# Performance work log

Hardware: AMD Instinct MI355X
Metric: run time of the kernel (lower is better)

## Reference

```python
import jax, jax.numpy as jnp
import numpy as np

NX = NY = 128
N = NX * NY            # 16384 tiles
F = 26                 # in_feats
H = 512                # hidden_dim
NH = 8                 # heads
HD = H // NH           # head_dim = 64
DEPTH = 4
LN_EPS = 1e-5


def _grid_edge_index(nx, ny):
    """4-connected grid, bidirectional edges (src, dst) like _build_grid_edge_index."""
    idx = np.arange(nx * ny).reshape(nx, ny)
    hs, hd = idx[:, :-1].ravel(), idx[:, 1:].ravel()   # horizontal neighbors
    vs, vd = idx[:-1, :].ravel(), idx[1:, :].ravel()   # vertical neighbors
    src = np.concatenate([hs, hd, vs, vd]).astype(np.int32)
    dst = np.concatenate([hd, hs, vd, vs]).astype(np.int32)
    return src, dst


def setup_inputs() -> dict:
    key = jax.random.key(0)
    ks = jax.random.split(key, 8)
    s = 0.02
    src, dst = _grid_edge_index(NX, NY)
    return {
        "graph": jax.random.normal(ks[0], (N, F), jnp.float32),
        "edge_src": jnp.asarray(src),
        "edge_dst": jnp.asarray(dst),
        "Wp": jax.random.normal(ks[1], (F, H), jnp.float32) * s,
        "bp": jnp.zeros((H,), jnp.float32),
        "Wq": jax.random.normal(ks[2], (DEPTH, H, H), jnp.float32) * s,
        "bq": jnp.zeros((DEPTH, H), jnp.float32),
        "Wk": jax.random.normal(ks[3], (DEPTH, H, H), jnp.float32) * s,
        "bk": jnp.zeros((DEPTH, H), jnp.float32),
        "Wv": jax.random.normal(ks[4], (DEPTH, H, H), jnp.float32) * s,
        "bv": jnpp_zeros((DEPTH, H)) if False else jnp.zeros((DEPTH, H), jnp.float32),
        "Ws": jax.random.normal(ks[5], (DEPTH, H, H), jnp.float32) * s,
        "bs": jnp.zeros((DEPTH, H), jnp.float32),
        "Wbeta": jax.random.normal(ks[6], (DEPTH, 3 * H), jnp.float32) * s,
        "ln_g": jnp.ones((DEPTH, H), jnp.float32),
        "ln_b": jnp.zeros((DEPTH, H), jnp.float32),
    }


def _layernorm(x, g, b):
    mu = x.mean(-1, keepdims=True)
    var = ((x - mu) ** 2).mean(-1, keepdims=True)
    return (x - mu) * jax.lax.rsqrt(var + LN_EPS) * g + b


def _transformer_conv(x, src, dst, Wq, bq, Wk, bk, Wv, bv, Ws, bs, Wbeta):
    n = x.shape[0]
    q = (x @ Wq + bq).reshape(n, NH, HD)
    k = (x @ Wk + bk).reshape(n, NH, HD)
    v = (x @ Wv + bv).reshape(n, NH, HD)
    # per-edge attention logits: query at target (dst), key at source (src)
    alpha = (q[dst] * k[src]).sum(-1) / jnp.sqrt(jnp.float32(HD))  # (E, NH)
    # segment softmax over incoming edges of each target node (PyG softmax)
    m = jax.ops.segment_max(alpha, dst, num_segments=n)
    e = jnp.exp(alpha - m[dst])
    denom = jax.ops.segment_sum(e, dst, num_segments=n)
    a = e / (denom[dst] + 1e-16)
    # beta-gated scatter-add aggregation
    out = jax.ops.segment_sum(a[:, :, None] * v[src], dst, num_segments=n)
    out = out.reshape(n, H)
    r = x @ Ws + bs                                  # root/skip projection
    g = jax.nn.sigmoid(jnp.concatenate([out, r, out - r], -1) @ Wbeta)  # (n,)
    g = g[:, None]
    return g * r + (1.0 - g) * out


def reference(graph, edge_src, edge_dst, Wp, bp, Wq, bq, Wk, bk, Wv, bv,
              Ws, bs, Wbeta, ln_g, ln_b):
    x = graph @ Wp + bp
    for l in range(DEPTH):
        h = _transformer_conv(x, edge_src, edge_dst, Wq[l], bq[l], Wk[l], bk[l],
                              Wv[l], bv[l], Ws[l], bs[l], Wbeta[l])
        x = _layernorm(x + h, ln_g[l], ln_b[l])
    global_emb = x.mean(0, keepdims=True)
    return (x, global_emb)


def jnp_zeros(shape):  # unused helper guard
    return jnp.zeros(shape, jnp.float32)

jnp_p_zeros = None

def jnp_zeros_unused():
    pass

# fix accidental typo-safe alias used in setup_inputs
jnp_zeros_f = jnp.zeros

def jnp_noop():
    pass

jnp_zeros2 = jnp.zeros

def jnp_p_zeros_fn(shape):
    return jnp.zeros(shape, jnp.float32)

jnp_p_zeros = jnp_p_zeros_fn

def jnp_zeros3(shape):
    return jnp.zeros(shape, jnp.float32)

jnp_p = jnp

def jnp_zeros4(shape):
    return jnp.zeros(shape, jnp.float32)

jnp_zeros5 = jnp.zeros

def jnp_zeros6(shape):
    return jnp.zeros(shape, jnp.float32)

jnp_p_zeros_alias = jnp.zeros

def jnp_p_zeros_(shape):
    return jnp.zeros(shape, jnp.float32)

jnp_p_zeros__ = jnp.zeros

# alias referenced defensively inside setup_inputs (never called)
jnp_p_zeros___ = jnp.zeros

def jnp_p_zeros____(shape):
    return jnp.zeros(shape, jnp.float32)

jnp_p_zeros_____ = jnp.zeros

jnp_p_zeros______ = jnp.zeros

jnp_p_zeros_______ = jnp.zeros

jnp_p_zeros________ = jnp.zeros

jnp_p_zeros_________ = jnp.zeros

jnp_p_zeros__________ = jnp.zeros

# name used in the dead branch of setup_inputs
jnp_p_zeros = jnp.zeros

def jnp_p_zeros_def(shape):
    return jnp.zeros(shape, jnp.float32)

jnpp_zeros = jnp.zeros
```

## Files before the change

kernel.cpp:

```cpp
#include <hip/hip_runtime.h>
#include <hip/hip_bf16.h>
#include <math.h>

#define NN    16384
#define FF    26
#define HH    512
#define NHEAD 8
#define HDIM  64
#define GRID_W 128
#define LN_EPS 1e-5f

typedef __attribute__((ext_vector_type(8))) short short8;
typedef __attribute__((ext_vector_type(4))) float f32x4;
typedef __attribute__((ext_vector_type(4))) short s16x4;

static __device__ __forceinline__ float bf2f(short u) {
  unsigned int x = ((unsigned int)(unsigned short)u) << 16;
  return __uint_as_float(x);
}
static __device__ __forceinline__ short f2bf(float f) {
  __hip_bfloat16 h = __float2bfloat16(f);
  return __builtin_bit_cast(short, h);
}
static __device__ __forceinline__ float dot8(short8 a, short8 b) {
  float p = 0.f;
#pragma unroll
  for (int j = 0; j < 8; ++j) p += bf2f(a[j]) * bf2f(b[j]);
  return p;
}

__global__ __launch_bounds__(256) void wconv_kernel(
    const float* __restrict__ Wq, const float* __restrict__ Wk,
    const float* __restrict__ Wv, const float* __restrict__ Ws,
    __hip_bfloat16* __restrict__ Wt) {
  __shared__ float ls[32][33];
  int bid = blockIdx.x;
  int mi = bid >> 8, kt = (bid >> 4) & 15, nt = bid & 15;
  int l = mi >> 2, m = mi & 3;
  const float* src = ((m == 0) ? Wq : (m == 1) ? Wk : (m == 2) ? Wv : Ws)
                   + (size_t)l * 262144;
  int c = threadIdx.x & 31, r = threadIdx.x >> 5;
#pragma unroll
  for (int p = 0; p < 4; ++p)
    ls[r + 8 * p][c] = src[(size_t)(kt * 32 + r + 8 * p) * 512 + nt * 32 + c];
  __syncthreads();
#pragma unroll
  for (int p = 0; p < 4; ++p)
    Wt[((size_t)mi * 512 + nt * 32 + r + 8 * p) * 512 + kt * 32 + c] =
        __float2bfloat16(ls[c][r + 8 * p]);
}

__global__ __launch_bounds__(256) void bconv_kernel(
    const float* __restrict__ bq, const float* __restrict__ bk,
    const float* __restrict__ bv, const float* __restrict__ bs,
    float* __restrict__ bcat) {
  int tid = blockIdx.x * 256 + threadIdx.x;
  int j = tid & 511;
  int m = (tid >> 9) & 3;
  int l = tid >> 11;
  const float* src = (m == 0) ? bq : (m == 1) ? bk : (m == 2) ? bv : bs;
  bcat[tid] = src[l * 512 + j];
}

__global__ __launch_bounds__(256) void gconv_kernel(
    const float* __restrict__ graph, __hip_bfloat16* __restrict__ gb) {
  int tid = blockIdx.x * 256 + threadIdx.x;
  int n = tid >> 5, k = tid & 31;
  gb[tid] = __float2bfloat16(k < FF ? graph[n * FF + k] : 0.f);
}

__global__ __launch_bounds__(256) void wpconv_kernel(
    const float* __restrict__ Wp, __hip_bfloat16* __restrict__ Wpt) {
  int tid = blockIdx.x * 256 + threadIdx.x;
  int j = tid >> 5, k = tid & 31;
  Wpt[tid] = __float2bfloat16(k < FF ? Wp[k * HH + j] : 0.f);
}

template <int LDA, int KDIM, int LDC, bool WF32, bool REPACK>
__global__ __launch_bounds__(256) void gemm_t(
    const __hip_bfloat16* __restrict__ A,
    const __hip_bfloat16* __restrict__ Bt,
    const float* __restrict__ bias,
    __hip_bfloat16* __restrict__ C,
    float* __restrict__ Xf) {
  __shared__ __align__(16) char lds[16384];
  const int t    = threadIdx.x;
  const int wv   = t >> 6;
  const int lane = t & 63;
  const int m0 = blockIdx.x * 128, n0 = blockIdx.y * 128;

  const int srow = (wv << 4) + (lane >> 2);
  const int gch  = (lane & 3) ^ ((lane >> 3) & 3);
  const char* agp = (const char*)(A  + (size_t)(m0 + srow) * LDA + (gch << 3));
  const char* bgp = (const char*)(Bt + (size_t)(n0 + srow) * KDIM + (gch << 3));
  char* aldst = lds +        (wv << 10) + (lane << 4);
  char* bldst = lds + 8192 + (wv << 10) + (lane << 4);

  const int q  = lane >> 4;
  const int r  = lane & 15;
  const int fs = (r >> 1) & 3;
  const int ksl = ((q ^ fs) << 4);
  const int wm = wv >> 1, wn = wv & 1;
  int aoff[4], boff[4];
#pragma unroll
  for (int i = 0; i < 4; ++i) {
    aoff[i] = (((wm << 6) + (i << 4) + r) << 6) + ksl;
    boff[i] = 8192 + (((wn << 6) + (i << 4) + r) << 6) + ksl;
  }

  f32x4 acc[4][4];
#pragma unroll
  for (int i = 0; i < 4; ++i)
#pragma unroll
    for (int j = 0; j < 4; ++j) acc[i][j] = (f32x4){0.f, 0.f, 0.f, 0.f};

  for (int k0 = 0; k0 < KDIM; k0 += 32) {
    __syncthreads();
    const size_t kb = (size_t)k0 * 2;
    __builtin_amdgcn_global_load_lds(
        (const __attribute__((address_space(1))) void*)(agp + kb),
        (__attribute__((address_space(3))) void*)(aldst), 16, 0, 0);
    __builtin_amdgcn_global_load_lds(
        (const __attribute__((address_space(1))) void*)(agp + kb + (size_t)LDA * 128),
        (__attribute__((address_space(3))) void*)(aldst + 4096), 16, 0, 0);
    __builtin_amdgcn_global_load_lds(
        (const __attribute__((address_space(1))) void*)(bgp + kb),
        (__attribute__((address_space(3))) void*)(bldst), 16, 0, 0);
    __builtin_amdgcn_global_load_lds(
        (const __attribute__((address_space(1))) void*)(bgp + kb + (size_t)KDIM * 128),
        (__attribute__((address_space(3))) void*)(bldst + 4096), 16, 0, 0);
    __syncthreads();

    short8 af[4], bfr[4];
#pragma unroll
    for (int i = 0; i < 4; ++i) af[i]  = *(const short8*)(lds + aoff[i]);
#pragma unroll
    for (int i = 0; i < 4; ++i) bfr[i] = *(const short8*)(lds + boff[i]);
#pragma unroll
    for (int mi = 0; mi < 4; ++mi)
#pragma unroll
      for (int ni = 0; ni < 4; ++ni)
        acc[mi][ni] = __builtin_amdgcn_mfma_f32_16x16x32_bf16(
            af[mi], bfr[ni], acc[mi][ni], 0, 0, 0);
  }

  if (REPACK) {
    const int S = 136;
    short* lp = (short*)lds;
#pragma unroll
    for (int mi = 0; mi < 4; ++mi) {
      __syncthreads();
#pragma unroll
      for (int ni = 0; ni < 4; ++ni) {
        const int col = (wn << 6) + (ni << 4) + r;
        const float bb = bias[n0 + col];
#pragma unroll
        for (int e = 0; e < 4; ++e)
          lp[((wm << 4) + (q << 2) + e) * S + col] = f2bf(acc[mi][ni][e] + bb);
      }
      __syncthreads();
#pragma unroll
      for (int s2 = 0; s2 < 2; ++s2) {
        const int slot = t + (s2 << 8);
        const int rl = slot >> 4, seg = slot & 15;
        short8 vseg = *(const short8*)(lp + rl * S + (seg << 3));
        const int grow = m0 + ((rl >> 4) << 6) + (mi << 4) + (rl & 15);
        *(short8*)(C + (size_t)grow * LDC + n0 + (seg << 3)) = vseg;
      }
    }
  } else {
#pragma unroll
    for (int ni = 0; ni < 4; ++ni) {
      const int col = n0 + (wn << 6) + (ni << 4) + r;
      const float bb = bias[col];
#pragma unroll
      for (int mi = 0; mi < 4; ++mi) {
        const size_t rb = (size_t)(m0 + (wm << 6) + (mi << 4) + (q << 2));
#pragma unroll
        for (int e = 0; e < 4; ++e) {
          float val = acc[mi][ni][e] + bb;
          C[(rb + e) * LDC + col] = __float2bfloat16(val);
          if (WF32) Xf[(rb + e) * LDC + col] = val;
        }
      }
    }
  }
}

__global__ __launch_bounds__(128) void node_kernel(
    const __hip_bfloat16* __restrict__ qkvs,
    float* __restrict__ x, __hip_bfloat16* __restrict__ xb,
    const float* __restrict__ Wb, const float* __restrict__ lng,
    const float* __restrict__ lnb) {
  int n = blockIdx.x;
  int t = threadIdx.x;
  __shared__ float s_alpha[32];
  __shared__ float s_aw[32];
  __shared__ float redA[2], redB[2], redC[2];

  const int gi = n >> 7, gj = n & 127;
  int nbr[4];
  nbr[0] = (gj > 0)          ? n - 1      : -1;
  nbr[1] = (gj < GRID_W - 1) ? n + 1      : -1;
  nbr[2] = (gi > 0)          ? n - GRID_W : -1;
  nbr[3] = (gi < GRID_W - 1) ? n + GRID_W : -1;

  {
    const int e = t >> 5, h = (t >> 2) & 7, sub = t & 3;
    const int me = (nbr[e] >= 0) ? nbr[e] : n;
    const short8* qp = (const short8*)(qkvs + (size_t)n * 2048 + h * 64 + sub * 16);
    const short8* kp = (const short8*)(qkvs + (size_t)me * 2048 + 512 + h * 64 + sub * 16);
    float p = dot8(qp[0], kp[0]) + dot8(qp[1], kp[1]);
    p += __shfl_xor(p, 1);
    p += __shfl_xor(p, 2);
    if (sub == 0) s_alpha[e * 8 + h] = p * 0.125f;
  }
  __syncthreads();

  if (t < 8) {
    float a[4];
#pragma unroll
    for (int e = 0; e < 4; ++e) a[e] = (nbr[e] >= 0) ? s_alpha[e * 8 + t] : -1e30f;
    float mx = fmaxf(fmaxf(a[0], a[1]), fmaxf(a[2], a[3]));
    float ee[4];
    float sum = 1e-16f;
#pragma unroll
    for (int e = 0; e < 4; ++e) {
      ee[e] = (nbr[e] >= 0) ? expf(a[e] - mx) : 0.f;
      sum += ee[e];
    }
    float inv = 1.f / sum;
#pragma unroll
    for (int e = 0; e < 4; ++e) s_aw[t * 4 + e] = ee[e] * inv;
  }
  __syncthreads();

  const int c0 = t << 2;
  const int h  = c0 >> 6;

  float4 ov = make_float4(0.f, 0.f, 0.f, 0.f);
#pragma unroll
  for (int e = 0; e < 4; ++e) {
    int m = nbr[e];
    if (m >= 0) {
      float a = s_aw[h * 4 + e];
      s16x4 vv = *(const s16x4*)(qkvs + (size_t)m * 2048 + 1024 + c0);
      ov.x += a * bf2f(vv[0]); ov.y += a * bf2f(vv[1]);
      ov.z += a * bf2f(vv[2]); ov.w += a * bf2f(vv[3]);
    }
  }
  s16x4 rr = *(const s16x4*)(qkvs + (size_t)n * 2048 + 1536 + c0);
  float4 rv = make_float4(bf2f(rr[0]), bf2f(rr[1]), bf2f(rr[2]), bf2f(rr[3]));

  float4 w0 = *(const float4*)(Wb + c0);
  float4 w1 = *(const float4*)(Wb + 512 + c0);
  float4 w2 = *(const float4*)(Wb + 1024 + c0);
  float part = ov.x * w0.x + ov.y * w0.y + ov.z * w0.z + ov.w * w0.w
             + rv.x * w1.x + rv.y * w1.y + rv.z * w1.z + rv.w * w1.w
             + (ov.x - rv.x) * w2.x + (ov.y - rv.y) * w2.y
             + (ov.z - rv.z) * w2.z + (ov.w - rv.w) * w2.w;
#pragma unroll
  for (int s = 32; s > 0; s >>= 1) part += __shfl_xor(part, s);
  int wv = t >> 6, ln = t & 63;
  if (ln == 0) redA[wv] = part;
  __syncthreads();
  float g = 1.f / (1.f + expf(-(redA[0] + redA[1])));

  float4 xv = *(const float4*)(x + (size_t)n * HH + c0);
  float4 y;
  y.x = xv.x + g * rv.x + (1.f - g) * ov.x;
  y.y = xv.y + g * rv.y + (1.f - g) * ov.y;
  y.z = xv.z + g * rv.z + (1.f - g) * ov.z;
  y.w = xv.w + g * rv.w + (1.f - g) * ov.w;

  float s1 = y.x + y.y + y.z + y.w;
  float sq = y.x * y.x + y.y * y.y + y.z * y.z + y.w * y.w;
#pragma unroll
  for (int s = 32; s > 0; s >>= 1) {
    s1 += __shfl_xor(s1, s);
    sq += __shfl_xor(sq, s);
  }
  if (ln == 0) { redB[wv] = s1; redC[wv] = sq; }
  __syncthreads();
  float S1 = redB[0] + redB[1], S2 = redC[0] + redC[1];
  float mu  = S1 * (1.f / 512.f);
  float var = S2 * (1.f / 512.f) - mu * mu;
  float rs  = rsqrtf(var + LN_EPS);

  float4 gg = *(const float4*)(lng + c0);
  float4 bb = *(const float4*)(lnb + c0);
  float4 o;
  o.x = (y.x - mu) * rs * gg.x + bb.x;
  o.y = (y.y - mu) * rs * gg.y + bb.y;
  o.z = (y.z - mu) * rs * gg.z + bb.z;
  o.w = (y.w - mu) * rs * gg.w + bb.w;
  *(float4*)(x + (size_t)n * HH + c0) = o;
  s16x4 ob;
  ob[0] = f2bf(o.x); ob[1] = f2bf(o.y); ob[2] = f2bf(o.z); ob[3] = f2bf(o.w);
  *(s16x4*)(xb + (size_t)n * HH + c0) = ob;
}

__global__ void zero_kernel(float* __restrict__ p) { p[threadIdx.x] = 0.f; }

__global__ __launch_bounds__(512) void col_mean_kernel(
    const float* __restrict__ x, float* __restrict__ g) {
  int t  = threadIdx.x;
  int n0 = blockIdx.x * 256;
  float s = 0.f;
  for (int rr = 0; rr < 256; ++rr) s += x[(size_t)(n0 + rr) * HH + t];
  atomicAdd(&g[t], s * (1.f / 16384.f));
}

extern "C" void kernel_launch(void* const* d_in, const int* in_sizes, int n_in,
                              void* d_out, int out_size, void* d_ws, size_t ws_size,
                              hipStream_t stream) {
  const float* graph = (const float*)d_in[0];
  const float* Wp = (const float*)d_in[3];
  const float* bp = (const float*)d_in[4];
  const float* Wq = (const float*)d_in[5];
  const float* bq = (const float*)d_in[6];
  const float* Wk = (const float*)d_in[7];
  const float* bk = (const float*)d_in[8];
  const float* Wv = (const float*)d_in[9];
  const float* bv = (const float*)d_in[10];
  const float* Wst = (const float*)d_in[11];
  const float* bst = (const float*)d_in[12];
  const float* Wbeta = (const float*)d_in[13];
  const float* lng = (const float*)d_in[14];
  const float* lnb = (const float*)d_in[15];

  float* x = (float*)d_out;
  char* ws = (char*)d_ws;
  __hip_bfloat16* qkvs = (__hip_bfloat16*)ws;
  __hip_bfloat16* xb   = (__hip_bfloat16*)(ws + 67108864);
  __hip_bfloat16* Wt   = (__hip_bfloat16*)(ws + 83886080);
  __hip_bfloat16* gb   = (__hip_bfloat16*)(ws + 92274688);
  __hip_bfloat16* Wpt  = (__hip_bfloat16*)(ws + 93323264);
  float* bcat          = (float*)(ws + 93356032);

  wconv_kernel<<<4096, 256, 0, stream>>>(Wq, Wk, Wv, Wst, Wt);
  bconv_kernel<<<32, 256, 0, stream>>>(bq, bk, bv, bst, bcat);
  gconv_kernel<<<NN * 32 / 256, 256, 0, stream>>>(graph, gb);
  wpconv_kernel<<<64, 256, 0, stream>>>(Wp, Wpt);

  gemm_t<32, 32, 512, true, false><<<dim3(128, 4), 256, 0, stream>>>(
      gb, Wpt, bp, xb, x);

  for (int l = 0; l < 4; ++l) {
    gemm_t<512, 512, 2048, false, true><<<dim3(128, 16), 256, 0, stream>>>(
        xb, Wt + (size_t)l * 4 * 262144, bcat + l * 2048, qkvs, nullptr);
    node_kernel<<<NN, 128, 0, stream>>>(qkvs, x, xb,
        Wbeta + (size_t)l * 1536, lng + (size_t)l * 512, lnb + (size_t)l * 512);
  }

  zero_kernel<<<1, 512, 0, stream>>>(x + (size_t)NN * HH);
  col_mean_kernel<<<64, 512, 0, stream>>>(x, x + (size_t)NN * HH);
}
```

Baseline: 448.6 us.

## Use per-wave GEMM epilogue repack and one-wave-per-node attention kernel

The GEMM epilogue now repacks each wave's 16x64 tile through its own LDS region and writes 16-byte rows. This replaces the block-wide repack, which needed a __syncthreads per row group. The node kernel maps one 64-lane wave to each node, with four nodes arranged as a 2x2 grid patch per block, so every reduction is done with wave shuffles and no LDS or barriers. The goal is to remove synchronisation overhead, widen loads to 8 bf16 per lane, and improve neighbour locality. The per-wave LDS repack uses a 66-element stride, which may cause bank conflicts.

```diff
diff --git a/kernel.cpp b/kernel.cpp
--- a/kernel.cpp
+++ b/kernel.cpp
@@ -76,7 +76,7 @@
   Wpt[tid] = __float2bfloat16(k < FF ? Wp[k * HH + j] : 0.f);
 }
 
-template <int LDA, int KDIM, int LDC, bool WF32, bool REPACK>
+template <int LDA, int KDIM, int LDC, bool WF32>
 __global__ __launch_bounds__(256) void gemm_t(
     const __hip_bfloat16* __restrict__ A,
     const __hip_bfloat16* __restrict__ Bt,
@@ -144,160 +144,151 @@
             af[mi], bfr[ni], acc[mi][ni], 0, 0, 0);
   }
 
-  if (REPACK) {
-    const int S = 136;
-    short* lp = (short*)lds;
-#pragma unroll
-    for (int mi = 0; mi < 4; ++mi) {
-      __syncthreads();
+  float bbv[4];
+#pragma unroll
+  for (int ni = 0; ni < 4; ++ni) bbv[ni] = bias[n0 + (wn << 6) + (ni << 4) + r];
+
+  __syncthreads();
+
+  short* lp = (short*)(lds + (wv << 12));
+  const int rl = lane >> 2, sg = lane & 3;
+#pragma unroll
+  for (int mi = 0; mi < 4; ++mi) {
+#pragma unroll
+    for (int ni = 0; ni < 4; ++ni)
+#pragma unroll
+      for (int e = 0; e < 4; ++e)
+        lp[((q << 2) + e) * 66 + (ni << 4) + r] = f2bf(acc[mi][ni][e] + bbv[ni]);
+    const short* rp = lp + rl * 66 + (sg << 4);
+    short8 v0 = *(const short8*)rp;
+    short8 v1 = *(const short8*)(rp + 8);
+    const int grow = m0 + (wm << 6) + (mi << 4) + rl;
+    short8* cp = (short8*)(C + (size_t)grow * LDC + n0 + (wn << 6) + (sg << 4));
+    cp[0] = v0;
+    cp[1] = v1;
+    if (WF32) {
 #pragma unroll
       for (int ni = 0; ni < 4; ++ni) {
-        const int col = (wn << 6) + (ni << 4) + r;
-        const float bb = bias[n0 + col];
+        const int col = n0 + (wn << 6) + (ni << 4) + r;
+        const size_t rb = (size_t)(m0 + (wm << 6) + (mi << 4) + (q << 2));
 #pragma unroll
         for (int e = 0; e < 4; ++e)
-          lp[((wm << 4) + (q << 2) + e) * S + col] = f2bf(acc[mi][ni][e] + bb);
-      }
-      __syncthreads();
-#pragma unroll
-      for (int s2 = 0; s2 < 2; ++s2) {
-        const int slot = t + (s2 << 8);
-        const int rl = slot >> 4, seg = slot & 15;
-        short8 vseg = *(const short8*)(lp + rl * S + (seg << 3));
-        const int grow = m0 + ((rl >> 4) << 6) + (mi << 4) + (rl & 15);
-        *(short8*)(C + (size_t)grow * LDC + n0 + (seg << 3)) = vseg;
+          Xf[(rb + e) * LDC + col] = acc[mi][ni][e] + bbv[ni];
       }
     }
-  } else {
-#pragma unroll
-    for (int ni = 0; ni < 4; ++ni) {
-      const int col = n0 + (wn << 6) + (ni << 4) + r;
-      const float bb = bias[col];
-#pragma unroll
-      for (int mi = 0; mi < 4; ++mi) {
-        const size_t rb = (size_t)(m0 + (wm << 6) + (mi << 4) + (q << 2));
-#pragma unroll
-        for (int e = 0; e < 4; ++e) {
-          float val = acc[mi][ni][e] + bb;
-          C[(rb + e) * LDC + col] = __float2bfloat16(val);
-          if (WF32) Xf[(rb + e) * LDC + col] = val;
-        }
-      }
-    }
-  }
-}
-
-__global__ __launch_bounds__(128) void node_kernel(
+  }
+}
+
+__global__ __launch_bounds__(256) void node_kernel(
     const __hip_bfloat16* __restrict__ qkvs,
     float* __restrict__ x, __hip_bfloat16* __restrict__ xb,
     const float* __restrict__ Wb, const float* __restrict__ lng,
     const float* __restrict__ lnb) {
-  int n = blockIdx.x;
-  int t = threadIdx.x;
-  __shared__ float s_alpha[32];
-  __shared__ float s_aw[32];
-  __shared__ float redA[2], redB[2], redC[2];
-
-  const int gi = n >> 7, gj = n & 127;
+  const int t = threadIdx.x;
+  const int wv = t >> 6, lane = t & 63;
+  const int bi = blockIdx.x;
+  const int gi = ((bi >> 6) << 1) + (wv >> 1);
+  const int gj = ((bi & 63) << 1) + (wv & 1);
+  const int n = (gi << 7) + gj;
+
   int nbr[4];
   nbr[0] = (gj > 0)          ? n - 1      : -1;
   nbr[1] = (gj < GRID_W - 1) ? n + 1      : -1;
   nbr[2] = (gi > 0)          ? n - GRID_W : -1;
   nbr[3] = (gi < GRID_W - 1) ? n + GRID_W : -1;
 
-  {
-    const int e = t >> 5, h = (t >> 2) & 7, sub = t & 3;
+  const int c0 = lane << 3;
+
+  short8 q8 = *(const short8*)(qkvs + (size_t)n * 2048 + c0);
+  float al[4];
+#pragma unroll
+  for (int e = 0; e < 4; ++e) {
     const int me = (nbr[e] >= 0) ? nbr[e] : n;
-    const short8* qp = (const short8*)(qkvs + (size_t)n * 2048 + h * 64 + sub * 16);
-    const short8* kp = (const short8*)(qkvs + (size_t)me * 2048 + 512 + h * 64 + sub * 16);
-    float p = dot8(qp[0], kp[0]) + dot8(qp[1], kp[1]);
+    short8 k8 = *(const short8*)(qkvs + (size_t)me * 2048 + 512 + c0);
+    float p = dot8(q8, k8);
     p += __shfl_xor(p, 1);
     p += __shfl_xor(p, 2);
-    if (sub == 0) s_alpha[e * 8 + h] = p * 0.125f;
-  }
-  __syncthreads();
-
-  if (t < 8) {
-    float a[4];
-#pragma unroll
-    for (int e = 0; e < 4; ++e) a[e] = (nbr[e] >= 0) ? s_alpha[e * 8 + t] : -1e30f;
-    float mx = fmaxf(fmaxf(a[0], a[1]), fmaxf(a[2], a[3]));
-    float ee[4];
-    float sum = 1e-16f;
-#pragma unroll
-    for (int e = 0; e < 4; ++e) {
-      ee[e] = (nbr[e] >= 0) ? expf(a[e] - mx) : 0.f;
-      sum += ee[e];
+    p += __shfl_xor(p, 4);
+    al[e] = (nbr[e] >= 0) ? p * 0.125f : -1e30f;
+  }
+  float mx = fmaxf(fmaxf(al[0], al[1]), fmaxf(al[2], al[3]));
+  float aw[4], sum = 1e-16f;
+#pragma unroll
+  for (int e = 0; e < 4; ++e) {
+    aw[e] = (nbr[e] >= 0) ? expf(al[e] - mx) : 0.f;
+    sum += aw[e];
+  }
+  float inv = 1.f / sum;
+#pragma unroll
+  for (int e = 0; e < 4; ++e) aw[e] *= inv;
+
+  float ov[8] = {0.f, 0.f, 0.f, 0.f, 0.f, 0.f, 0.f, 0.f};
+#pragma unroll
+  for (int e = 0; e < 4; ++e) {
+    if (nbr[e] >= 0) {
+      short8 v8 = *(const short8*)(qkvs + (size_t)nbr[e] * 2048 + 1024 + c0);
+#pragma unroll
+      for (int j = 0; j < 8; ++j) ov[j] += aw[e] * bf2f(v8[j]);
     }
-    float inv = 1.f / sum;
-#pragma unroll
-    for (int e = 0; e < 4; ++e) s_aw[t * 4 + e] = ee[e] * inv;
-  }
-  __syncthreads();
-
-  const int c0 = t << 2;
-  const int h  = c0 >> 6;
-
-  float4 ov = make_float4(0.f, 0.f, 0.f, 0.f);
-#pragma unroll
-  for (int e = 0; e < 4; ++e) {
-    int m = nbr[e];
-    if (m >= 0) {
-      float a = s_aw[h * 4 + e];
-      s16x4 vv = *(const s16x4*)(qkvs + (size_t)m * 2048 + 1024 + c0);
-      ov.x += a * bf2f(vv[0]); ov.y += a * bf2f(vv[1]);
-      ov.z += a * bf2f(vv[2]); ov.w += a * bf2f(vv[3]);
-    }
-  }
-  s16x4 rr = *(const s16x4*)(qkvs + (size_t)n * 2048 + 1536 + c0);
-  float4 rv = make_float4(bf2f(rr[0]), bf2f(rr[1]), bf2f(rr[2]), bf2f(rr[3]));
-
-  float4 w0 = *(const float4*)(Wb + c0);
-  float4 w1 = *(const float4*)(Wb + 512 + c0);
-  float4 w2 = *(const float4*)(Wb + 1024 + c0);
-  float part = ov.x * w0.x + ov.y * w0.y + ov.z * w0.z + ov.w * w0.w
-             + rv.x * w1.x + rv.y * w1.y + rv.z * w1.z + rv.w * w1.w
-             + (ov.x - rv.x) * w2.x + (ov.y - rv.y) * w2.y
-             + (ov.z - rv.z) * w2.z + (ov.w - rv.w) * w2.w;
+  }
+  short8 s8 = *(const short8*)(qkvs + (size_t)n * 2048 + 1536 + c0);
+  float rv[8];
+#pragma unroll
+  for (int j = 0; j < 8; ++j) rv[j] = bf2f(s8[j]);
+
+  const float4* w0p = (const float4*)(Wb + c0);
+  const float4* w1p = (const float4*)(Wb + 512 + c0);
+  const float4* w2p = (const float4*)(Wb + 1024 + c0);
+  float4 w0a = w0p[0], w0b = w0p[1];
+  float4 w1a = w1p[0], w1b = w1p[1];
+  float4 w2a = w2p[0], w2b = w2p[1];
+  float w0[8] = {w0a.x, w0a.y, w0a.z, w0a.w, w0b.x, w0b.y, w0b.z, w0b.w};
+  float w1[8] = {w1a.x, w1a.y, w1a.z, w1a.w, w1b.x, w1b.y, w1b.z, w1b.w};
+  float w2[8] = {w2a.x, w2a.y, w2a.z, w2a.w, w2b.x, w2b.y, w2b.z, w2b.w};
+  float part = 0.f;
+#pragma unroll
+  for (int j = 0; j < 8; ++j)
+    part += ov[j] * w0[j] + rv[j] * w1[j] + (ov[j] - rv[j]) * w2[j];
 #pragma unroll
   for (int s = 32; s > 0; s >>= 1) part += __shfl_xor(part, s);
-  int wv = t >> 6, ln = t & 63;
-  if (ln == 0) redA[wv] = part;
-  __syncthreads();
-  float g = 1.f / (1.f + expf(-(redA[0] + redA[1])));
-
-  float4 xv = *(const float4*)(x + (size_t)n * HH + c0);
-  float4 y;
-  y.x = xv.x + g * rv.x + (1.f - g) * ov.x;
-  y.y = xv.y + g * rv.y + (1.f - g) * ov.y;
-  y.z = xv.z + g * rv.z + (1.f - g) * ov.z;
-  y.w = xv.w + g * rv.w + (1.f - g) * ov.w;
-
-  float s1 = y.x + y.y + y.z + y.w;
-  float sq = y.x * y.x + y.y * y.y + y.z * y.z + y.w * y.w;
+  float g = 1.f / (1.f + expf(-part));
+
+  const float4* xp = (const float4*)(x + (size_t)n * HH + c0);
+  float4 xa = xp[0], xc = xp[1];
+  float xv[8] = {xa.x, xa.y, xa.z, xa.w, xc.x, xc.y, xc.z, xc.w};
+  float y[8], s1 = 0.f, sq = 0.f;
+#pragma unroll
+  for (int j = 0; j < 8; ++j) {
+    y[j] = xv[j] + g * rv[j] + (1.f - g) * ov[j];
+    s1 += y[j];
+    sq += y[j] * y[j];
+  }
 #pragma unroll
   for (int s = 32; s > 0; s >>= 1) {
     s1 += __shfl_xor(s1, s);
     sq += __shfl_xor(sq, s);
   }
-  if (ln == 0) { redB[wv] = s1; redC[wv] = sq; }
-  __syncthreads();
-  float S1 = redB[0] + redB[1], S2 = redC[0] + redC[1];
-  float mu  = S1 * (1.f / 512.f);
-  float var = S2 * (1.f / 512.f) - mu * mu;
+  float mu  = s1 * (1.f / 512.f);
+  float var = sq * (1.f / 512.f) - mu * mu;
   float rs  = rsqrtf(var + LN_EPS);
 
-  float4 gg = *(const float4*)(lng + c0);
-  float4 bb = *(const float4*)(lnb + c0);
-  float4 o;
-  o.x = (y.x - mu) * rs * gg.x + bb.x;
-  o.y = (y.y - mu) * rs * gg.y + bb.y;
-  o.z = (y.z - mu) * rs * gg.z + bb.z;
-  o.w = (y.w - mu) * rs * gg.w + bb.w;
-  *(float4*)(x + (size_t)n * HH + c0) = o;
-  s16x4 ob;
-  ob[0] = f2bf(o.x); ob[1] = f2bf(o.y); ob[2] = f2bf(o.z); ob[3] = f2bf(o.w);
-  *(s16x4*)(xb + (size_t)n * HH + c0) = ob;
+  const float4* gp = (const float4*)(lng + c0);
+  const float4* bp = (const float4*)(lnb + c0);
+  float4 ga = gp[0], gc = gp[1];
+  float4 ba = bp[0], bc = bp[1];
+  float gg[8] = {ga.x, ga.y, ga.z, ga.w, gc.x, gc.y, gc.z, gc.w};
+  float bb[8] = {ba.x, ba.y, ba.z, ba.w, bc.x, bc.y, bc.z, bc.w};
+  float o[8];
+  short8 ob;
+#pragma unroll
+  for (int j = 0; j < 8; ++j) {
+    o[j] = (y[j] - mu) * rs * gg[j] + bb[j];
+    ob[j] = f2bf(o[j]);
+  }
+  float4* xo = (float4*)(x + (size_t)n * HH + c0);
+  xo[0] = make_float4(o[0], o[1], o[2], o[3]);
+  xo[1] = make_float4(o[4], o[5], o[6], o[7]);
+  *(short8*)(xb + (size_t)n * HH + c0) = ob;
 }
 
 __global__ void zero_kernel(float* __restrict__ p) { p[threadIdx.x] = 0.f; }
@@ -343,13 +334,13 @@
   gconv_kernel<<<NN * 32 / 256, 256, 0, stream>>>(graph, gb);
   wpconv_kernel<<<64, 256, 0, stream>>>(Wp, Wpt);
 
-  gemm_t<32, 32, 512, true, false><<<dim3(128, 4), 256, 0, stream>>>(
+  gemm_t<32, 32, 512, true><<<dim3(128, 4), 256, 0, stream>>>(
       gb, Wpt, bp, xb, x);
 
   for (int l = 0; l < 4; ++l) {
-    gemm_t<512, 512, 2048, false, true><<<dim3(128, 16), 256, 0, stream>>>(
+    gemm_t<512, 512, 2048, false><<<dim3(128, 16), 256, 0, stream>>>(
         xb, Wt + (size_t)l * 4 * 262144, bcat + l * 2048, qkvs, nullptr);
-    node_kernel<<<NN, 128, 0, stream>>>(qkvs, x, xb,
+    node_kernel<<<4096, 256, 0, stream>>>(qkvs, x, xb,
         Wbeta + (size_t)l * 1536, lng + (size_t)l * 512, lnb + (size_t)l * 512);
   }
 
```

Result: faster. 436.2 us (-2.8%).
